# Kernel optimization log

Measured on AMD Instinct MI355X. Metric: run time of the kernel, lower is better.

## Reference

```python
import jax, jax.numpy as jnp
import numpy as np

EPS = 1e-8  # torch.cosine_similarity default eps


def setup_inputs() -> dict:
    key = jax.random.key(0)
    k1, k2, k3 = jax.random.split(key, 3)
    B, N, M, C = 8, 2048, 2048, 128
    z = jax.random.randint(k1, (B, N, M), 0, 3, dtype=jnp.int32) - 1  # values in {-1,0,1}
    x1 = jax.random.normal(k2, (B, N, C), dtype=jnp.float32)
    x2 = jax.random.normal(k3, (B, M, C), dtype=jnp.float32)
    s = 10.0
    t = jnp.asarray(s, dtype=jnp.float32)   # nn.Parameter(s)
    b = jnp.asarray(-s, dtype=jnp.float32)  # nn.Parameter(-s)
    return {"z": z, "x1": x1, "x2": x2, "t": t, "b": b}


def reference(z, x1, x2, t, b):
    # cosine similarity as a GEMM instead of broadcast O(B*N*M*C) product:
    # cos = (x1 . x2) / max(||x1|| * ||x2||, eps)  (matches torch.cosine_similarity)
    dots = jnp.einsum('bnc,bmc->bnm', x1, x2)            # [B,N,M]
    n1 = jnp.sqrt(jnp.sum(x1 * x1, axis=-1))             # [B,N]
    n2 = jnp.sqrt(jnp.sum(x2 * x2, axis=-1))             # [B,M]
    denom = jnp.maximum(n1[:, :, None] * n2[:, None, :], EPS)
    cos_sim = dots / denom                               # [B,N,M]

    y = z.astype(jnp.float32) * (t * cos_sim - b)
    mask = z != 0
    nll = -jax.nn.log_sigmoid(y)
    loss = jnp.sum(jnp.where(mask, nll, 0.0)) / jnp.sum(mask).astype(jnp.float32)
    return loss, cos_sim, mask
```

## Files before the change

### kernel.cpp

```cpp
#include <hip/hip_runtime.h>
#include <hip/hip_bf16.h>

#define BATCH 8
#define NDIM  2048
#define MDIM  2048
#define CDIM  128

typedef __attribute__((ext_vector_type(8))) short bf16x8;
typedef __attribute__((ext_vector_type(4))) float f32x4;
typedef __attribute__((ext_vector_type(4), aligned(4))) float f32x4u;

__device__ __forceinline__ float bf2f(unsigned int u16){
    union { unsigned int u; float f; } v; v.u = u16 << 16; return v.f;
}
__device__ __forceinline__ unsigned int f2bf(float f){
    union { float f; unsigned int u; } v; v.f = f;
    unsigned int u = v.u;
    u += 0x7FFFu + ((u >> 16) & 1u);
    return u >> 16;
}

__device__ __forceinline__ void gload_lds16(const void* g, void* l){
    __builtin_amdgcn_global_load_lds(
        (const __attribute__((address_space(1))) void*)g,
        (__attribute__((address_space(3))) void*)l, 16, 0, 0);
}

__global__ void finalize_kernel(const float* cells, float* out){
    float s = 0.f;
    int   c = 0;
    #pragma unroll
    for (int i = 0; i < 32; ++i){
        s += cells[i];
        c += ((const int*)cells)[32 + i];
    }
    out[0] = s / (float)c;
}

__global__ __launch_bounds__(256) void prep_kernel(
    const float* __restrict__ x1, const float* __restrict__ x2,
    unsigned short* __restrict__ xb, float* __restrict__ inv,
    unsigned int* __restrict__ cells)
{
    if (blockIdx.x == 0 && threadIdx.x < 64) cells[threadIdx.x] = 0u;

    int gt  = blockIdx.x*256 + threadIdx.x;
    int row = gt >> 4;
    int seg = gt & 15;
    const float* src = (row < 16384) ? (x1 + (size_t)row*128)
                                     : (x2 + (size_t)(row - 16384)*128);
    float4 a = *(const float4*)(src + seg*8);
    float4 b = *(const float4*)(src + seg*8 + 4);
    uint4 pk;
    pk.x = f2bf(a.x) | (f2bf(a.y) << 16);
    pk.y = f2bf(a.z) | (f2bf(a.w) << 16);
    pk.z = f2bf(b.x) | (f2bf(b.y) << 16);
    pk.w = f2bf(b.z) | (f2bf(b.w) << 16);
    ((uint4*)xb)[(size_t)row*16 + seg] = pk;

    float f0 = bf2f(pk.x & 0xffffu), f1 = bf2f(pk.x >> 16);
    float f2 = bf2f(pk.y & 0xffffu), f3 = bf2f(pk.y >> 16);
    float f4 = bf2f(pk.z & 0xffffu), f5 = bf2f(pk.z >> 16);
    float f6 = bf2f(pk.w & 0xffffu), f7 = bf2f(pk.w >> 16);
    float s = f0*f0 + f1*f1 + f2*f2 + f3*f3 + f4*f4 + f5*f5 + f6*f6 + f7*f7;
    s += __shfl_xor(s, 1);
    s += __shfl_xor(s, 2);
    s += __shfl_xor(s, 4);
    s += __shfl_xor(s, 8);
    if (seg == 0) inv[row] = 1.0f / sqrtf(fmaxf(s, 1e-16f));
}

__global__ __launch_bounds__(256, 5) void cossim_bce_fast(
    const int*  __restrict__ zp,
    const unsigned short* __restrict__ xb,
    const float* __restrict__ inv,
    const float* __restrict__ tparm,
    const float* __restrict__ bparm,
    float* __restrict__ out,
    float* __restrict__ cells)
{
    __shared__ __align__(16) unsigned short lB[128*128];

    const int t  = threadIdx.x;
    const int bx = blockIdx.x;
    const int by = blockIdx.y;
    const int bz = blockIdx.z;

    const float tv = *tparm;
    const float bv = *bparm;

    const unsigned short* x1b = xb;
    const unsigned short* x2b = xb + (size_t)16384*128;
    const int x1r0 = bz*NDIM + by*64;
    const int x2r0 = bz*MDIM + bx*128;

    const int lane = t & 63;
    const int w    = t >> 6;
    const int quad = lane >> 4;
    const int l16  = lane & 15;
    const int hi   = lane >> 5;
    const int c4   = lane & 31;

    f32x4 acc[8];
    #pragma unroll
    for (int n = 0; n < 8; ++n)
        acc[n] = (f32x4){0.f, 0.f, 0.f, 0.f};

    const size_t rowBase = (size_t)bz*NDIM*MDIM + (size_t)(by*64 + w*16)*MDIM + (size_t)(bx*128);

    int4 zpre[4];
    #pragma unroll
    for (int i = 0; i < 4; ++i)
        zpre[i] = *(const int4*)(zp + rowBase + (size_t)(i*4 + hi)*MDIM + c4*4);

    #pragma unroll
    for (int i = 0; i < 8; ++i){
        int chunk = i*256 + t;
        int row = chunk >> 4, pp = chunk & 15;
        int srcpos = pp ^ (row & 7);
        gload_lds16(x2b + ((size_t)(x2r0 + row))*128 + srcpos*8,
                    lB + (size_t)(i*256 + w*64)*8);
    }
    __syncthreads();

    const unsigned short* aRow = x1b + ((size_t)(x1r0 + w*16 + l16))*128 + quad*8;
    #pragma unroll
    for (int kk = 0; kk < 4; ++kk){
        bf16x8 afr = *(const bf16x8*)(aRow + kk*32);
        const int kc = kk*4 + quad;
        #pragma unroll
        for (int g = 0; g < 2; ++g){
            bf16x8 bfr[4];
            #pragma unroll
            for (int nn = 0; nn < 4; ++nn){
                int brow = (g*4 + nn)*16 + l16;
                bfr[nn] = ((const bf16x8*)lB)[brow*16 + (kc ^ (brow & 7))];
            }
            #pragma unroll
            for (int nn = 0; nn < 4; ++nn)
                acc[g*4+nn] = __builtin_amdgcn_mfma_f32_16x16x32_bf16(
                                afr, bfr[nn], acc[g*4+nn], 0, 0, 0);
        }
    }

    float in1[4], in2[8];
    #pragma unroll
    for (int r = 0; r < 4; ++r) in1[r] = inv[x1r0 + w*16 + quad*4 + r];
    #pragma unroll
    for (int n = 0; n < 8; ++n) in2[n] = inv[16384 + x2r0 + n*16 + l16];

    __syncthreads();

    float* scr = (float*)lB + w*1024;
    float* cosOut  = out + 1;
    float* maskOut = out + 1 + (size_t)BATCH*NDIM*MDIM;

    float lnum = 0.f;
    int   lcnt = 0;

    #pragma unroll
    for (int rr = 0; rr < 2; ++rr){
        #pragma unroll
        for (int n = 0; n < 8; ++n){
            #pragma unroll
            for (int j = 0; j < 2; ++j){
                int r  = rr*2 + j;
                int sr = quad*2 + j;
                scr[sr*128 + ((n*16 + l16 + sr*4) & 127)] = acc[n][r] * in1[r] * in2[n];
            }
        }
        #pragma unroll
        for (int i = 0; i < 4; ++i){
            int sr  = i*2 + hi;
            int col = (c4*4 + sr*4) & 127;
            f32x4 cs4 = *(const f32x4*)(scr + sr*128 + col);
            int rowRel = i*4 + rr*2 + hi;
            size_t idx = rowBase + (size_t)rowRel*MDIM + c4*4;

            int4 z4 = zpre[i];
            if (rr == 0)
                zpre[i] = *(const int4*)(zp + idx + (size_t)2*MDIM);

            f32x4 mk;
            float nl = 0.f;
            int   nc = 0;
            #pragma unroll
            for (int j = 0; j < 4; ++j){
                int zv = (&z4.x)[j];
                float cs = cs4[j];
                mk[j] = zv ? 1.0f : 0.0f;
                float y  = (float)zv * (tv*cs - bv);
                float nll = fmaxf(-y, 0.f) + __logf(1.0f + __expf(-fabsf(y)));
                nl += zv ? nll : 0.f;
                nc += zv ? 1 : 0;
            }
            lnum += nl;
            lcnt += nc;
            *(f32x4u*)(cosOut  + idx) = cs4;
            *(f32x4u*)(maskOut + idx) = mk;
        }
    }

    #pragma unroll
    for (int off = 32; off > 0; off >>= 1){
        lnum += __shfl_down(lnum, off);
        lcnt += __shfl_down(lcnt, off);
    }
    __syncthreads();
    float* redf = (float*)lB;
    int*   redi = (int*)lB + 8;
    if (lane == 0){ redf[w] = lnum; redi[w] = lcnt; }
    __syncthreads();
    if (t == 0){
        float s = redf[0] + redf[1] + redf[2] + redf[3];
        int   c = redi[0] + redi[1] + redi[2] + redi[3];
        int cell = (bx + by*16 + bz*512) & 31;
        atomicAdd(cells + cell, s);
        atomicAdd((int*)cells + 32 + cell, c);
    }
}

__global__ void ws_init_kernel(unsigned int* cells){
    cells[threadIdx.x] = 0u;
}

__global__ __launch_bounds__(256, 5) void cossim_bce_main(
    const int*  __restrict__ zp,
    const float* __restrict__ x1,
    const float* __restrict__ x2,
    const float* __restrict__ tparm,
    const float* __restrict__ bparm,
    float* __restrict__ out,
    float* __restrict__ wsf)
{
    __shared__ __align__(16) unsigned short lds[(64 + 128) * 64];
    __shared__ float nsh[192];
    unsigned short* lA = lds;
    unsigned short* lB = lds + 64*64;

    const int t  = threadIdx.x;
    const int bx = blockIdx.x;
    const int by = blockIdx.y;
    const int bz = blockIdx.z;

    const float tv = *tparm;
    const float bv = *bparm;

    const float* x1base = x1 + ((size_t)(bz*NDIM) + by*64 ) * CDIM;
    const float* x2base = x2 + ((size_t)(bz*MDIM) + bx*128) * CDIM;

    const int lane = t & 63;
    const int w    = t >> 6;
    const int quad = lane >> 4;
    const int l16  = lane & 15;
    const int hi   = lane >> 5;
    const int c4   = lane & 31;

    f32x4 acc[8];
    #pragma unroll
    for (int n = 0; n < 8; ++n)
        acc[n] = (f32x4){0.f, 0.f, 0.f, 0.f};

    float nsum = 0.f;

    #pragma unroll
    for (int ph = 0; ph < 2; ++ph){
        #pragma unroll
        for (int i = 0; i < 6; ++i){
            int chunk = i*256 + t;
            const float* srcb;
            uint4* dst;
            int row, pos;
            if (i < 2){
                row = chunk >> 3; pos = chunk & 7;
                srcb = x1base; dst = (uint4*)lA;
            } else {
                int c2 = chunk - 512;
                row = c2 >> 3; pos = c2 & 7;
                srcb = x2base; dst = (uint4*)lB;
            }
            const float* p = srcb + row*CDIM + ph*64 + pos*8;
            float4 a = *(const float4*)p;
            float4 b = *(const float4*)(p + 4);
            uint4 pk;
            pk.x = f2bf(a.x) | (f2bf(a.y) << 16);
            pk.y = f2bf(a.z) | (f2bf(a.w) << 16);
            pk.z = f2bf(b.x) | (f2bf(b.y) << 16);
            pk.w = f2bf(b.z) | (f2bf(b.w) << 16);
            dst[row*8 + (pos ^ (row & 7))] = pk;
        }
        __syncthreads();

        #pragma unroll
        for (int kk = 0; kk < 2; ++kk){
            const int kc = kk*4 + quad;
            const int arow = w*16 + l16;
            bf16x8 afr = ((const bf16x8*)lA)[arow*8 + (kc ^ (arow & 7))];
            #pragma unroll
            for (int g = 0; g < 2; ++g){
                bf16x8 bfr[4];
                #pragma unroll
                for (int nn = 0; nn < 4; ++nn){
                    int brow = (g*4 + nn)*16 + l16;
                    bfr[nn] = ((const bf16x8*)lB)[brow*8 + (kc ^ (brow & 7))];
                }
                #pragma unroll
                for (int nn = 0; nn < 4; ++nn)
                    acc[g*4+nn] = __builtin_amdgcn_mfma_f32_16x16x32_bf16(
                                    afr, bfr[nn], acc[g*4+nn], 0, 0, 0);
            }
        }

        if (t < 192){
            const uint4* base; int row;
            if (t < 64){ base = (const uint4*)lA; row = t; }
            else       { base = (const uint4*)lB; row = t - 64; }
            #pragma unroll
            for (int c = 0; c < 8; ++c){
                uint4 v = base[row*8 + (c ^ (row & 7))];
                float f0 = bf2f(v.x & 0xffffu), f1 = bf2f(v.x >> 16);
                float f2 = bf2f(v.y & 0xffffu), f3 = bf2f(v.y >> 16);
                float f4 = bf2f(v.z & 0xffffu), f5 = bf2f(v.z >> 16);
                float f6 = bf2f(v.w & 0xffffu), f7 = bf2f(v.w >> 16);
                nsum += f0*f0 + f1*f1 + f2*f2 + f3*f3 + f4*f4 + f5*f5 + f6*f6 + f7*f7;
            }
        }
        __syncthreads();
    }

    if (t < 192) nsh[t] = 1.0f / sqrtf(fmaxf(nsum, 1e-16f));
    __syncthreads();

    float in1[4], in2[8];
    #pragma unroll
    for (int r = 0; r < 4; ++r) in1[r] = nsh[w*16 + quad*4 + r];
    #pragma unroll
    for (int n = 0; n < 8; ++n) in2[n] = nsh[64 + n*16 + l16];

    float* scr = (float*)lds + w*1024;
    float* cosOut  = out + 1;
    float* maskOut = out + 1 + (size_t)BATCH*NDIM*MDIM;
    const size_t rowBase = (size_t)bz*NDIM*MDIM + (size_t)(by*64 + w*16)*MDIM + (size_t)(bx*128);

    float lnum = 0.f;
    int   lcnt = 0;

    int4 zpre[4];
    #pragma unroll
    for (int i = 0; i < 4; ++i)
        zpre[i] = *(const int4*)(zp + rowBase + (size_t)(i*4 + hi)*MDIM + c4*4);

    #pragma unroll
    for (int rr = 0; rr < 2; ++rr){
        #pragma unroll
        for (int n = 0; n < 8; ++n){
            #pragma unroll
            for (int j = 0; j < 2; ++j){
                int r  = rr*2 + j;
                int sr = quad*2 + j;
                scr[sr*128 + ((n*16 + l16 + sr*4) & 127)] = acc[n][r] * in1[r] * in2[n];
            }
        }
        #pragma unroll
        for (int i = 0; i < 4; ++i){
            int sr  = i*2 + hi;
            int col = (c4*4 + sr*4) & 127;
            f32x4 cs4 = *(const f32x4*)(scr + sr*128 + col);
            int rowRel = i*4 + rr*2 + hi;
            size_t idx = rowBase + (size_t)rowRel*MDIM + c4*4;

            int4 z4 = zpre[i];
            if (rr == 0)
                zpre[i] = *(const int4*)(zp + idx + (size_t)2*MDIM);

            f32x4 mk;
            float nl = 0.f;
            int   nc = 0;
            #pragma unroll
            for (int j = 0; j < 4; ++j){
                int zv = (&z4.x)[j];
                float cs = cs4[j];
                mk[j] = zv ? 1.0f : 0.0f;
                float y  = (float)zv * (tv*cs - bv);
                float nll = fmaxf(-y, 0.f) + __logf(1.0f + __expf(-fabsf(y)));
                nl += zv ? nll : 0.f;
                nc += zv ? 1 : 0;
            }
            lnum += nl;
            lcnt += nc;
            *(f32x4u*)(cosOut  + idx) = cs4;
            *(f32x4u*)(maskOut + idx) = mk;
        }
    }

    #pragma unroll
    for (int off = 32; off > 0; off >>= 1){
        lnum += __shfl_down(lnum, off);
        lcnt += __shfl_down(lcnt, off);
    }
    __syncthreads();
    if (lane == 0){ nsh[w] = lnum; ((int*)nsh)[4 + w] = lcnt; }
    __syncthreads();
    if (t == 0){
        float s = nsh[0] + nsh[1] + nsh[2] + nsh[3];
        int   c = ((int*)nsh)[4] + ((int*)nsh)[5] + ((int*)nsh)[6] + ((int*)nsh)[7];
        int cell = (bx + by*16 + bz*512) & 31;
        atomicAdd(wsf + cell, s);
        atomicAdd((int*)wsf + 32 + cell, c);
    }
}

extern "C" void kernel_launch(void* const* d_in, const int* in_sizes, int n_in,
                              void* d_out, int out_size, void* d_ws, size_t ws_size,
                              hipStream_t stream) {
    const int*   zp = (const int*)  d_in[0];
    const float* x1 = (const float*)d_in[1];
    const float* x2 = (const float*)d_in[2];
    const float* tp = (const float*)d_in[3];
    const float* bp = (const float*)d_in[4];
    float* out = (float*)d_out;

    const size_t WS_NEEDED = (size_t)8*1024*1024 + 32768*4 + 256;
    dim3 grid(MDIM/128, NDIM/64, BATCH);

    if (ws_size >= WS_NEEDED){
        unsigned short* xb  = (unsigned short*)d_ws;
        float* inv   = (float*)((char*)d_ws + (size_t)8*1024*1024);
        float* cells = inv + 32768;
        prep_kernel<<<2048, 256, 0, stream>>>(x1, x2, xb, inv, (unsigned int*)cells);
        cossim_bce_fast<<<grid, 256, 0, stream>>>(zp, xb, inv, tp, bp, out, cells);
        finalize_kernel<<<1, 1, 0, stream>>>(cells, out);
    } else {
        float* wsf = (float*)d_ws;
        ws_init_kernel<<<1, 64, 0, stream>>>((unsigned int*)d_ws);
        cossim_bce_main<<<grid, 256, 0, stream>>>(zp, x1, x2, tp, bp, out, wsf);
        finalize_kernel<<<1, 1, 0, stream>>>(wsf, out);
    }
}
```

Baseline: 118.6 us.

## Reuse staged x2 tile across four row tiles per block with prefetching

Each block now keeps its 128-row x2 tile in LDS and loops over four 64-row x1 tiles, so the grid shrinks 4x along N. The x1 fragments for the next iteration and the z values for the next tile are prefetched during the epilogue, and a separate LDS scratch region lets the GEMM and the writeback avoid sharing the B buffer. This cuts redundant x2 loads and block launch overhead in a kernel that is mostly bound by output bandwidth. In exchange it lowers occupancy (launch bounds 5 to 3, larger LDS) and puts fewer blocks in flight.

```diff
diff --git a/kernel.cpp b/kernel.cpp
--- a/kernel.cpp
+++ b/kernel.cpp
@@ -70,7 +70,7 @@
     if (seg == 0) inv[row] = 1.0f / sqrtf(fmaxf(s, 1e-16f));
 }
 
-__global__ __launch_bounds__(256, 5) void cossim_bce_fast(
+__global__ __launch_bounds__(256, 3) void cossim_bce_fast(
     const int*  __restrict__ zp,
     const unsigned short* __restrict__ xb,
     const float* __restrict__ inv,
@@ -79,11 +79,11 @@
     float* __restrict__ out,
     float* __restrict__ cells)
 {
-    __shared__ __align__(16) unsigned short lB[128*128];
+    __shared__ __align__(16) unsigned short lds[128*128 + 8192];
 
     const int t  = threadIdx.x;
     const int bx = blockIdx.x;
-    const int by = blockIdx.y;
+    const int g  = blockIdx.y;
     const int bz = blockIdx.z;
 
     const float tv = *tparm;
@@ -91,7 +91,6 @@
 
     const unsigned short* x1b = xb;
     const unsigned short* x2b = xb + (size_t)16384*128;
-    const int x1r0 = bz*NDIM + by*64;
     const int x2r0 = bz*MDIM + bx*128;
 
     const int lane = t & 63;
@@ -101,17 +100,14 @@
     const int hi   = lane >> 5;
     const int c4   = lane & 31;
 
-    f32x4 acc[8];
-    #pragma unroll
-    for (int n = 0; n < 8; ++n)
-        acc[n] = (f32x4){0.f, 0.f, 0.f, 0.f};
-
-    const size_t rowBase = (size_t)bz*NDIM*MDIM + (size_t)(by*64 + w*16)*MDIM + (size_t)(bx*128);
-
+    unsigned short* lB = lds;
+    float* scr = (float*)(lds + 128*128) + w*1024;
+
+    const size_t rowBase0 = (size_t)bz*NDIM*MDIM + (size_t)(g*256 + w*16)*MDIM + (size_t)(bx*128);
     int4 zpre[4];
     #pragma unroll
     for (int i = 0; i < 4; ++i)
-        zpre[i] = *(const int4*)(zp + rowBase + (size_t)(i*4 + hi)*MDIM + c4*4);
+        zpre[i] = *(const int4*)(zp + rowBase0 + (size_t)(i*4 + hi)*MDIM + c4*4);
 
     #pragma unroll
     for (int i = 0; i < 8; ++i){
@@ -121,37 +117,19 @@
         gload_lds16(x2b + ((size_t)(x2r0 + row))*128 + srcpos*8,
                     lB + (size_t)(i*256 + w*64)*8);
     }
-    __syncthreads();
-
-    const unsigned short* aRow = x1b + ((size_t)(x1r0 + w*16 + l16))*128 + quad*8;
-    #pragma unroll
-    for (int kk = 0; kk < 4; ++kk){
-        bf16x8 afr = *(const bf16x8*)(aRow + kk*32);
-        const int kc = kk*4 + quad;
-        #pragma unroll
-        for (int g = 0; g < 2; ++g){
-            bf16x8 bfr[4];
-            #pragma unroll
-            for (int nn = 0; nn < 4; ++nn){
-                int brow = (g*4 + nn)*16 + l16;
-                bfr[nn] = ((const bf16x8*)lB)[brow*16 + (kc ^ (brow & 7))];
-            }
-            #pragma unroll
-            for (int nn = 0; nn < 4; ++nn)
-                acc[g*4+nn] = __builtin_amdgcn_mfma_f32_16x16x32_bf16(
-                                afr, bfr[nn], acc[g*4+nn], 0, 0, 0);
-        }
-    }
-
-    float in1[4], in2[8];
-    #pragma unroll
-    for (int r = 0; r < 4; ++r) in1[r] = inv[x1r0 + w*16 + quad*4 + r];
+
+    float in2[8];
     #pragma unroll
     for (int n = 0; n < 8; ++n) in2[n] = inv[16384 + x2r0 + n*16 + l16];
 
-    __syncthreads();
-
-    float* scr = (float*)lB + w*1024;
+    const int aRowIdx = bz*NDIM + g*256 + w*16 + l16;
+    bf16x8 aCur[4];
+    #pragma unroll
+    for (int kk = 0; kk < 4; ++kk)
+        aCur[kk] = *(const bf16x8*)(x1b + (size_t)aRowIdx*128 + kk*32 + quad*8);
+
+    __syncthreads();
+
     float* cosOut  = out + 1;
     float* maskOut = out + 1 + (size_t)BATCH*NDIM*MDIM;
 
@@ -159,45 +137,86 @@
     int   lcnt = 0;
 
     #pragma unroll
-    for (int rr = 0; rr < 2; ++rr){
-        #pragma unroll
-        for (int n = 0; n < 8; ++n){
-            #pragma unroll
-            for (int j = 0; j < 2; ++j){
-                int r  = rr*2 + j;
-                int sr = quad*2 + j;
-                scr[sr*128 + ((n*16 + l16 + sr*4) & 127)] = acc[n][r] * in1[r] * in2[n];
-            }
-        }
-        #pragma unroll
-        for (int i = 0; i < 4; ++i){
-            int sr  = i*2 + hi;
-            int col = (c4*4 + sr*4) & 127;
-            f32x4 cs4 = *(const f32x4*)(scr + sr*128 + col);
-            int rowRel = i*4 + rr*2 + hi;
-            size_t idx = rowBase + (size_t)rowRel*MDIM + c4*4;
-
-            int4 z4 = zpre[i];
-            if (rr == 0)
-                zpre[i] = *(const int4*)(zp + idx + (size_t)2*MDIM);
-
-            f32x4 mk;
-            float nl = 0.f;
-            int   nc = 0;
-            #pragma unroll
-            for (int j = 0; j < 4; ++j){
-                int zv = (&z4.x)[j];
-                float cs = cs4[j];
-                mk[j] = zv ? 1.0f : 0.0f;
-                float y  = (float)zv * (tv*cs - bv);
-                float nll = fmaxf(-y, 0.f) + __logf(1.0f + __expf(-fabsf(y)));
-                nl += zv ? nll : 0.f;
-                nc += zv ? 1 : 0;
-            }
-            lnum += nl;
-            lcnt += nc;
-            *(f32x4u*)(cosOut  + idx) = cs4;
-            *(f32x4u*)(maskOut + idx) = mk;
+    for (int it = 0; it < 4; ++it){
+        const size_t rowBase = rowBase0 + (size_t)(it*64)*MDIM;
+
+        f32x4 acc[8];
+        #pragma unroll
+        for (int n = 0; n < 8; ++n)
+            acc[n] = (f32x4){0.f, 0.f, 0.f, 0.f};
+        #pragma unroll
+        for (int kk = 0; kk < 4; ++kk){
+            bf16x8 afr = aCur[kk];
+            const int kc = kk*4 + quad;
+            #pragma unroll
+            for (int g2 = 0; g2 < 2; ++g2){
+                bf16x8 bfr[4];
+                #pragma unroll
+                for (int nn = 0; nn < 4; ++nn){
+                    int brow = (g2*4 + nn)*16 + l16;
+                    bfr[nn] = ((const bf16x8*)lB)[brow*16 + (kc ^ (brow & 7))];
+                }
+                #pragma unroll
+                for (int nn = 0; nn < 4; ++nn)
+                    acc[g2*4+nn] = __builtin_amdgcn_mfma_f32_16x16x32_bf16(
+                                    afr, bfr[nn], acc[g2*4+nn], 0, 0, 0);
+            }
+        }
+
+        float in1[4];
+        #pragma unroll
+        for (int r = 0; r < 4; ++r)
+            in1[r] = inv[bz*NDIM + g*256 + it*64 + w*16 + quad*4 + r];
+
+        #pragma unroll
+        for (int rr = 0; rr < 2; ++rr){
+            #pragma unroll
+            for (int n = 0; n < 8; ++n){
+                #pragma unroll
+                for (int j = 0; j < 2; ++j){
+                    int r  = rr*2 + j;
+                    int sr = quad*2 + j;
+                    scr[sr*128 + ((n*16 + l16 + sr*4) & 127)] = acc[n][r] * in1[r] * in2[n];
+                }
+            }
+            if (rr == 0 && it < 3){
+                #pragma unroll
+                for (int kk = 0; kk < 4; ++kk)
+                    aCur[kk] = *(const bf16x8*)(x1b + (size_t)(aRowIdx + (it+1)*64)*128 + kk*32 + quad*8);
+            }
+            #pragma unroll
+            for (int i = 0; i < 4; ++i){
+                int sr  = i*2 + hi;
+                int col = (c4*4 + sr*4) & 127;
+                f32x4 cs4 = *(const f32x4*)(scr + sr*128 + col);
+                int rowRel = i*4 + rr*2 + hi;
+                size_t idx = rowBase + (size_t)rowRel*MDIM + c4*4;
+
+                int4 z4 = zpre[i];
+                if (rr == 0){
+                    zpre[i] = *(const int4*)(zp + idx + (size_t)2*MDIM);
+                } else if (it < 3){
+                    zpre[i] = *(const int4*)(zp + idx + (size_t)62*MDIM);
+                }
+
+                f32x4 mk;
+                float nl = 0.f;
+                int   nc = 0;
+                #pragma unroll
+                for (int j = 0; j < 4; ++j){
+                    int zv = (&z4.x)[j];
+                    float cs = cs4[j];
+                    mk[j] = zv ? 1.0f : 0.0f;
+                    float y  = (float)zv * (tv*cs - bv);
+                    float nll = fmaxf(-y, 0.f) + __logf(1.0f + __expf(-fabsf(y)));
+                    nl += zv ? nll : 0.f;
+                    nc += zv ? 1 : 0;
+                }
+                lnum += nl;
+                lcnt += nc;
+                *(f32x4u*)(cosOut  + idx) = cs4;
+                *(f32x4u*)(maskOut + idx) = mk;
+            }
         }
     }
 
@@ -207,14 +226,14 @@
         lcnt += __shfl_down(lcnt, off);
     }
     __syncthreads();
-    float* redf = (float*)lB;
-    int*   redi = (int*)lB + 8;
+    float* redf = (float*)(lds + 128*128);
+    int*   redi = (int*)(lds + 128*128) + 8;
     if (lane == 0){ redf[w] = lnum; redi[w] = lcnt; }
     __syncthreads();
     if (t == 0){
         float s = redf[0] + redf[1] + redf[2] + redf[3];
         int   c = redi[0] + redi[1] + redi[2] + redi[3];
-        int cell = (bx + by*16 + bz*512) & 31;
+        int cell = (bx + g*16 + bz*128) & 31;
         atomicAdd(cells + cell, s);
         atomicAdd((int*)cells + 32 + cell, c);
     }
@@ -421,18 +440,19 @@
     float* out = (float*)d_out;
 
     const size_t WS_NEEDED = (size_t)8*1024*1024 + 32768*4 + 256;
-    dim3 grid(MDIM/128, NDIM/64, BATCH);
 
     if (ws_size >= WS_NEEDED){
         unsigned short* xb  = (unsigned short*)d_ws;
         float* inv   = (float*)((char*)d_ws + (size_t)8*1024*1024);
         float* cells = inv + 32768;
         prep_kernel<<<2048, 256, 0, stream>>>(x1, x2, xb, inv, (unsigned int*)cells);
+        dim3 grid(MDIM/128, 8, BATCH);
         cossim_bce_fast<<<grid, 256, 0, stream>>>(zp, xb, inv, tp, bp, out, cells);
         finalize_kernel<<<1, 1, 0, stream>>>(cells, out);
     } else {
         float* wsf = (float*)d_ws;
         ws_init_kernel<<<1, 64, 0, stream>>>((unsigned int*)d_ws);
+        dim3 grid(MDIM/128, NDIM/64, BATCH);
         cossim_bce_main<<<grid, 256, 0, stream>>>(zp, x1, x2, tp, bp, out, wsf);
         finalize_kernel<<<1, 1, 0, stream>>>(wsf, out);
     }
```

New measurement: 138.8 us. 17.1% more time.

## Split each 64x128 tile across 8 waves and use base-2 log-sigmoid

Applied to the files above, without the earlier changes.

The fast kernel now launches 512 threads per block. Each row-group of 16 is split across two waves that each compute half of the 128 columns. This halves the accumulators and register pressure per wave, so more waves can be resident to hide the z loads and the cos/mask store traffic. The whole fp32 tile is staged in LDS in one pass instead of two half passes, and all z rows are prefetched up front. The log-sigmoid is rewritten with exp2/log2 and pre-scaled constants, with one multiply by ln2 at the end.

```diff
diff --git a/kernel.cpp b/kernel.cpp
--- a/kernel.cpp
+++ b/kernel.cpp
@@ -70,7 +70,7 @@
     if (seg == 0) inv[row] = 1.0f / sqrtf(fmaxf(s, 1e-16f));
 }
 
-__global__ __launch_bounds__(256, 5) void cossim_bce_fast(
+__global__ __launch_bounds__(512, 6) void cossim_bce_fast(
     const int*  __restrict__ zp,
     const unsigned short* __restrict__ xb,
     const float* __restrict__ inv,
@@ -86,72 +86,85 @@
     const int by = blockIdx.y;
     const int bz = blockIdx.z;
 
-    const float tv = *tparm;
-    const float bv = *bparm;
+    const float t2 = *tparm * 1.44269504f;
+    const float b2 = *bparm * 1.44269504f;
 
     const unsigned short* x1b = xb;
     const unsigned short* x2b = xb + (size_t)16384*128;
-    const int x1r0 = bz*NDIM + by*64;
     const int x2r0 = bz*MDIM + bx*128;
 
     const int lane = t & 63;
     const int w    = t >> 6;
+    const int wip  = w & 1;
+    const int pr   = w >> 1;
     const int quad = lane >> 4;
     const int l16  = lane & 15;
     const int hi   = lane >> 5;
     const int c4   = lane & 31;
 
-    f32x4 acc[8];
-    #pragma unroll
-    for (int n = 0; n < 8; ++n)
+    f32x4 acc[4];
+    #pragma unroll
+    for (int n = 0; n < 4; ++n)
         acc[n] = (f32x4){0.f, 0.f, 0.f, 0.f};
 
-    const size_t rowBase = (size_t)bz*NDIM*MDIM + (size_t)(by*64 + w*16)*MDIM + (size_t)(bx*128);
+    const size_t rowBase = (size_t)bz*NDIM*MDIM + (size_t)(by*64 + pr*16)*MDIM + (size_t)(bx*128);
 
     int4 zpre[4];
     #pragma unroll
     for (int i = 0; i < 4; ++i)
-        zpre[i] = *(const int4*)(zp + rowBase + (size_t)(i*4 + hi)*MDIM + c4*4);
-
-    #pragma unroll
-    for (int i = 0; i < 8; ++i){
-        int chunk = i*256 + t;
+        zpre[i] = *(const int4*)(zp + rowBase + (size_t)(i*4 + wip*2 + hi)*MDIM + c4*4);
+
+    #pragma unroll
+    for (int i = 0; i < 4; ++i){
+        int chunk = i*512 + t;
         int row = chunk >> 4, pp = chunk & 15;
         int srcpos = pp ^ (row & 7);
         gload_lds16(x2b + ((size_t)(x2r0 + row))*128 + srcpos*8,
-                    lB + (size_t)(i*256 + w*64)*8);
-    }
-    __syncthreads();
-
-    const unsigned short* aRow = x1b + ((size_t)(x1r0 + w*16 + l16))*128 + quad*8;
+                    lB + (size_t)(i*512 + w*64)*8);
+    }
+    __syncthreads();
+
+    const unsigned short* aRow = x1b + ((size_t)(bz*NDIM + by*64 + pr*16 + l16))*128 + quad*8;
     #pragma unroll
     for (int kk = 0; kk < 4; ++kk){
         bf16x8 afr = *(const bf16x8*)(aRow + kk*32);
         const int kc = kk*4 + quad;
         #pragma unroll
-        for (int g = 0; g < 2; ++g){
-            bf16x8 bfr[4];
-            #pragma unroll
-            for (int nn = 0; nn < 4; ++nn){
-                int brow = (g*4 + nn)*16 + l16;
+        for (int g2 = 0; g2 < 2; ++g2){
+            bf16x8 bfr[2];
+            #pragma unroll
+            for (int nn = 0; nn < 2; ++nn){
+                int brow = wip*64 + (g2*2 + nn)*16 + l16;
                 bfr[nn] = ((const bf16x8*)lB)[brow*16 + (kc ^ (brow & 7))];
             }
             #pragma unroll
-            for (int nn = 0; nn < 4; ++nn)
-                acc[g*4+nn] = __builtin_amdgcn_mfma_f32_16x16x32_bf16(
-                                afr, bfr[nn], acc[g*4+nn], 0, 0, 0);
-        }
-    }
-
-    float in1[4], in2[8];
-    #pragma unroll
-    for (int r = 0; r < 4; ++r) in1[r] = inv[x1r0 + w*16 + quad*4 + r];
-    #pragma unroll
-    for (int n = 0; n < 8; ++n) in2[n] = inv[16384 + x2r0 + n*16 + l16];
-
-    __syncthreads();
-
-    float* scr = (float*)lB + w*1024;
+            for (int nn = 0; nn < 2; ++nn)
+                acc[g2*2+nn] = __builtin_amdgcn_mfma_f32_16x16x32_bf16(
+                                afr, bfr[nn], acc[g2*2+nn], 0, 0, 0);
+        }
+    }
+
+    float in1[4], in2[4];
+    #pragma unroll
+    for (int r = 0; r < 4; ++r) in1[r] = inv[bz*NDIM + by*64 + pr*16 + quad*4 + r];
+    #pragma unroll
+    for (int n = 0; n < 4; ++n) in2[n] = inv[16384 + x2r0 + wip*64 + n*16 + l16];
+
+    __syncthreads();
+
+    float* scr = (float*)lB + pr*2048;
+
+    #pragma unroll
+    for (int n = 0; n < 4; ++n){
+        int col = wip*64 + n*16 + l16;
+        #pragma unroll
+        for (int r = 0; r < 4; ++r){
+            int row = quad*4 + r;
+            scr[row*128 + ((col + 4*row) & 127)] = acc[n][r] * in1[r] * in2[n];
+        }
+    }
+    __syncthreads();
+
     float* cosOut  = out + 1;
     float* maskOut = out + 1 + (size_t)BATCH*NDIM*MDIM;
 
@@ -159,47 +172,32 @@
     int   lcnt = 0;
 
     #pragma unroll
-    for (int rr = 0; rr < 2; ++rr){
-        #pragma unroll
-        for (int n = 0; n < 8; ++n){
-            #pragma unroll
-            for (int j = 0; j < 2; ++j){
-                int r  = rr*2 + j;
-                int sr = quad*2 + j;
-                scr[sr*128 + ((n*16 + l16 + sr*4) & 127)] = acc[n][r] * in1[r] * in2[n];
-            }
-        }
-        #pragma unroll
-        for (int i = 0; i < 4; ++i){
-            int sr  = i*2 + hi;
-            int col = (c4*4 + sr*4) & 127;
-            f32x4 cs4 = *(const f32x4*)(scr + sr*128 + col);
-            int rowRel = i*4 + rr*2 + hi;
-            size_t idx = rowBase + (size_t)rowRel*MDIM + c4*4;
-
-            int4 z4 = zpre[i];
-            if (rr == 0)
-                zpre[i] = *(const int4*)(zp + idx + (size_t)2*MDIM);
-
-            f32x4 mk;
-            float nl = 0.f;
-            int   nc = 0;
-            #pragma unroll
-            for (int j = 0; j < 4; ++j){
-                int zv = (&z4.x)[j];
-                float cs = cs4[j];
-                mk[j] = zv ? 1.0f : 0.0f;
-                float y  = (float)zv * (tv*cs - bv);
-                float nll = fmaxf(-y, 0.f) + __logf(1.0f + __expf(-fabsf(y)));
-                nl += zv ? nll : 0.f;
-                nc += zv ? 1 : 0;
-            }
-            lnum += nl;
-            lcnt += nc;
-            *(f32x4u*)(cosOut  + idx) = cs4;
-            *(f32x4u*)(maskOut + idx) = mk;
-        }
-    }
+    for (int i = 0; i < 4; ++i){
+        int row = i*4 + wip*2 + hi;
+        int col = (c4*4 + 4*row) & 127;
+        f32x4 cs4 = *(const f32x4*)(scr + row*128 + col);
+        size_t idx = rowBase + (size_t)row*MDIM + c4*4;
+
+        int4 z4 = zpre[i];
+        f32x4 mk;
+        float nl = 0.f;
+        int   nc = 0;
+        #pragma unroll
+        for (int j = 0; j < 4; ++j){
+            int zv = (&z4.x)[j];
+            float cs = cs4[j];
+            mk[j] = zv ? 1.0f : 0.0f;
+            float y2  = (float)zv * (t2*cs - b2);
+            float nll = fmaxf(-y2, 0.f) + log2f(1.0f + exp2f(-fabsf(y2)));
+            nl += zv ? nll : 0.f;
+            nc += zv ? 1 : 0;
+        }
+        lnum += nl;
+        lcnt += nc;
+        *(f32x4u*)(cosOut  + idx) = cs4;
+        *(f32x4u*)(maskOut + idx) = mk;
+    }
+    lnum *= 0.69314718f;
 
     #pragma unroll
     for (int off = 32; off > 0; off >>= 1){
@@ -208,12 +206,13 @@
     }
     __syncthreads();
     float* redf = (float*)lB;
-    int*   redi = (int*)lB + 8;
+    int*   redi = (int*)lB + 16;
     if (lane == 0){ redf[w] = lnum; redi[w] = lcnt; }
     __syncthreads();
     if (t == 0){
-        float s = redf[0] + redf[1] + redf[2] + redf[3];
-        int   c = redi[0] + redi[1] + redi[2] + redi[3];
+        float s = 0.f; int c = 0;
+        #pragma unroll
+        for (int k = 0; k < 8; ++k){ s += redf[k]; c += redi[k]; }
         int cell = (bx + by*16 + bz*512) & 31;
         atomicAdd(cells + cell, s);
         atomicAdd((int*)cells + 32 + cell, c);
@@ -421,18 +420,19 @@
     float* out = (float*)d_out;
 
     const size_t WS_NEEDED = (size_t)8*1024*1024 + 32768*4 + 256;
-    dim3 grid(MDIM/128, NDIM/64, BATCH);
 
     if (ws_size >= WS_NEEDED){
         unsigned short* xb  = (unsigned short*)d_ws;
         float* inv   = (float*)((char*)d_ws + (size_t)8*1024*1024);
         float* cells = inv + 32768;
         prep_kernel<<<2048, 256, 0, stream>>>(x1, x2, xb, inv, (unsigned int*)cells);
-        cossim_bce_fast<<<grid, 256, 0, stream>>>(zp, xb, inv, tp, bp, out, cells);
+        dim3 grid(MDIM/128, NDIM/64, BATCH);
+        cossim_bce_fast<<<grid, 512, 0, stream>>>(zp, xb, inv, tp, bp, out, cells);
         finalize_kernel<<<1, 1, 0, stream>>>(cells, out);
     } else {
         float* wsf = (float*)d_ws;
         ws_init_kernel<<<1, 64, 0, stream>>>((unsigned int*)d_ws);
+        dim3 grid(MDIM/128, NDIM/64, BATCH);
         cossim_bce_main<<<grid, 256, 0, stream>>>(zp, x1, x2, tp, bp, out, wsf);
         finalize_kernel<<<1, 1, 0, stream>>>(wsf, out);
     }
```

After: 121.5 us. +2.5%, slower.
